# Performance work log

Hardware: AMD Instinct MI355X
Metric: run time of the kernel (lower is better)

## Reference

```python
import jax, jax.numpy as jnp
import numpy as np

B, N = 4, 8192


def setup_inputs() -> dict:
    key = jax.random.key(0)
    k1, k2, k3 = jax.random.split(key, 3)
    pc_pred = jax.random.normal(k1, (B, N, 3), dtype=jnp.float32)
    pc_target = jax.random.normal(k2, (B, N, 3), dtype=jnp.float32)
    fbpp = jax.random.uniform(k3, (B,), dtype=jnp.float32)
    return {"pc_pred": pc_pred, "pc_target": pc_target, "fbpp": fbpp, "lam": 1}


def _chamfer(x, y):
    # x: (B, N, 3), y: (B, M, 3)
    x2 = jnp.sum(x * x, axis=-1)                     # (B, N)
    y2 = jnp.sum(y * y, axis=-1)                     # (B, M)
    xy = jnp.einsum('bnd,bmd->bnm', x, y)            # (B, N, M)
    d2 = jnp.maximum(x2[:, :, None] + y2[:, None, :] - 2.0 * xy, 0.0)
    cham_x = jnp.mean(jnp.min(d2, axis=2), axis=1)   # (B,) pred -> target
    cham_y = jnp.mean(jnp.min(d2, axis=1), axis=1)   # (B,) target -> pred
    return jnp.mean(cham_x + cham_y)                 # scalar (batch mean)


def reference(pc_pred, pc_target, fbpp, lam):
    d = _chamfer(pc_pred, pc_target)
    r = jnp.mean(fbpp)
    return d + lam * r
```

## Files before the change

kernel.cpp:

```cpp
#include <hip/hip_runtime.h>
#include <math.h>


typedef __attribute__((ext_vector_type(8)))  short  short8;
typedef __attribute__((ext_vector_type(16))) float  f32x16;

#define YS      4
#define RPB     256

#define MFMA2(da, db, A, B0, B1) \
    asm("v_mfma_f32_32x32x16_bf16 %0, %2, %3, 0\n\t" \
        "v_mfma_f32_32x32x16_bf16 %1, %2, %4, 0\n\t" \
        "s_nop 7\n\t" \
        "s_nop 7" \
        : "=&v"(da), "=&v"(db) \
        : "v"(A), "v"(B0), "v"(B1))

static inline int roundup_h(int v, int a) { return (v + a - 1) / a * a; }

static __device__ __forceinline__ unsigned short f2bf(float f) {
    union { float f; unsigned int u; } v; v.f = f;
    unsigned int r = v.u + 0x7FFFu + ((v.u >> 16) & 1u);
    return (unsigned short)(r >> 16);
}
static __device__ __forceinline__ float bf2f(unsigned short s) {
    union { unsigned int u; float f; } v; v.u = ((unsigned int)s) << 16;
    return v.f;
}
static __device__ __forceinline__ unsigned int pk2(unsigned short lo,
                                                   unsigned short hi) {
    return (unsigned int)lo | ((unsigned int)hi << 16);
}

static __device__ __forceinline__ float allmin32(float v) {
    union { float f; int i; } u, t;
    u.f = v;
    t.i = __builtin_amdgcn_update_dpp(u.i, u.i, 0xB1, 0xF, 0xF, false);
    u.f = fminf(u.f, t.f);
    t.i = __builtin_amdgcn_update_dpp(u.i, u.i, 0x4E, 0xF, 0xF, false);
    u.f = fminf(u.f, t.f);
    t.i = __builtin_amdgcn_update_dpp(u.i, u.i, 0x124, 0xF, 0xF, false);
    u.f = fminf(u.f, t.f);
    t.i = __builtin_amdgcn_update_dpp(u.i, u.i, 0x128, 0xF, 0xF, false);
    u.f = fminf(u.f, t.f);
    t.i = __builtin_amdgcn_ds_swizzle(u.i, 0x401F);
    u.f = fminf(u.f, t.f);
    return u.f;
}

__global__ __launch_bounds__(256) void pack_kernel(
    const float* __restrict__ pred, const float* __restrict__ targ,
    int B, int N, int M, int NpadP, int NpadT,
    unsigned short* __restrict__ aP, unsigned short* __restrict__ bP,
    unsigned short* __restrict__ aT, unsigned short* __restrict__ bT)
{
    const int padmax = (NpadP > NpadT) ? NpadP : NpadT;
    const int gid = blockIdx.x * 256 + threadIdx.x;
    if (gid >= B * padmax) return;
    const int b = gid / padmax, i = gid - b * padmax;

    for (int cloud = 0; cloud < 2; ++cloud) {
        const int cnt  = cloud ? M : N;
        const int npad = cloud ? NpadT : NpadP;
        if (i >= npad) continue;
        const float* src = (cloud ? targ : pred) +
                           ((size_t)b * cnt + min(i, cnt - 1)) * 3;
        unsigned short* A  = (cloud ? aT : aP) + ((size_t)b * npad + i) * 16;
        unsigned short* Bk = (cloud ? bT : bP) + (size_t)b * npad * 16;

        const float xs[3] = {src[0], src[1], src[2]};
        const float n2 = xs[0]*xs[0] + xs[1]*xs[1] + xs[2]*xs[2];
        unsigned short th[3], tl[3], yh[3], yl[3];
        #pragma unroll
        for (int c = 0; c < 3; ++c) {
            const float t = -2.0f * xs[c];
            th[c] = f2bf(t);     tl[c] = f2bf(t - bf2f(th[c]));
            yh[c] = f2bf(xs[c]); yl[c] = f2bf(xs[c] - bf2f(yh[c]));
        }
        const unsigned short n2h = f2bf(n2);
        const unsigned short n2l = f2bf(n2 - bf2f(n2h));
        const unsigned short ONE = 0x3F80;

        uint4 alo, ahi, blo, bhi;
        alo.x = pk2(th[0], th[1]); alo.y = pk2(th[2], tl[0]);
        alo.z = pk2(tl[1], tl[2]); alo.w = pk2(th[0], th[1]);
        ahi.x = pk2(th[2], tl[0]); ahi.y = pk2(tl[1], tl[2]);
        ahi.z = pk2(ONE,  ONE);    ahi.w = pk2(n2h,  n2l);
        blo.x = pk2(yh[0], yh[1]); blo.y = pk2(yh[2], yh[0]);
        blo.z = pk2(yh[1], yh[2]); blo.w = pk2(yl[0], yl[1]);
        bhi.x = pk2(yl[2], yl[0]); bhi.y = pk2(yl[1], yl[2]);
        bhi.z = pk2(n2h,  n2l);    bhi.w = pk2(ONE,  ONE);

        *(uint4*)(A)     = alo;  *(uint4*)(A + 8) = ahi;
        const size_t tb = (size_t)(i >> 5) * 64 + (i & 31);
        *(uint4*)(Bk + tb * 8)        = blo;
        *(uint4*)(Bk + (tb + 32) * 8) = bhi;
    }
}

__global__ __launch_bounds__(256, 4) void mfma_sweep(
    const unsigned short* __restrict__ aP, const unsigned short* __restrict__ bP,
    const unsigned short* __restrict__ aT, const unsigned short* __restrict__ bT,
    int B, int N, int M, int NpadP, int NpadT, int NpadMax,
    float* __restrict__ rowpart)
{
    const int tid  = threadIdx.x;
    const int w    = tid >> 6;
    const int lane = tid & 63;
    const int lc   = lane & 31, h = lane >> 5;

    const int SP = NpadMax / RPB;
    int t = blockIdx.x;
    const int sp  = t % SP;  t /= SP;
    const int js  = t % YS;  t /= YS;
    const int b   = t % B;   t /= B;
    const int dir = t;

    const unsigned short* Xp = (dir == 0) ? aP : aT;
    const unsigned short* Yp = (dir == 0) ? bT : bP;
    const int NpadX = (dir == 0) ? NpadP : NpadT;
    const int NpadY = (dir == 0) ? NpadT : NpadP;
    const int Nx    = (dir == 0) ? N : M;
    if (sp * RPB >= NpadX) return;

    const int TM  = NpadY / 32;
    const int nt0 = TM / YS;
    const int t0  = js * nt0;

    const int row0 = sp * RPB + w * 64;
    const size_t abase = ((size_t)b * NpadX + row0 + lc) * 16 + (size_t)h * 8;
    const short8 a0 = *reinterpret_cast<const short8*>(Xp + abase);
    const short8 a1 = *reinterpret_cast<const short8*>(Xp + abase + 32 * 16);

    f32x16 rm0, rm1;
    #pragma unroll
    for (int r = 0; r < 16; ++r) {
        rm0[r] = __builtin_inff(); rm1[r] = __builtin_inff();
    }

    const unsigned short* yp =
        Yp + (size_t)b * NpadY * 16 + (size_t)t0 * 512 + (size_t)lane * 8;
    short8 c0 = *reinterpret_cast<const short8*>(yp);
    short8 c1 = *reinterpret_cast<const short8*>(yp + 512);

    for (int j = 0; j < nt0; j += 2) {
        const short8 n0 = *reinterpret_cast<const short8*>(yp + 1024);
        const short8 n1 = *reinterpret_cast<const short8*>(yp + 1536);
        yp += 1024;
        __builtin_amdgcn_sched_barrier(0);
        {
            f32x16 da, db;
            MFMA2(da, db, a0, c0, c1);
            #pragma unroll
            for (int r = 0; r < 16; ++r)
                rm0[r] = fminf(fminf(da[r], db[r]), rm0[r]);
        }
        {
            f32x16 da, db;
            MFMA2(da, db, a1, c0, c1);
            #pragma unroll
            for (int r = 0; r < 16; ++r)
                rm1[r] = fminf(fminf(da[r], db[r]), rm1[r]);
        }
        c0 = n0; c1 = n1;
    }

    const size_t outb = (((size_t)dir * B + b) * YS + js) * (size_t)NpadMax;
    #pragma unroll
    for (int r = 0; r < 16; ++r) {
        const float v0 = allmin32(rm0[r]);
        const float v1 = allmin32(rm1[r]);
        if (lc == 0) {
            const int rr = (r & 3) + 8 * (r >> 2) + 4 * h;
            const int ra = row0 + rr, rb = row0 + 32 + rr;
            if (ra < Nx) rowpart[outb + ra] = v0;
            if (rb < Nx) rowpart[outb + rb] = v1;
        }
    }
}

__global__ __launch_bounds__(256) void combine_kernel(
    const float* __restrict__ rowpart, int B, int N, int M,
    int NpadP, int NpadT, int NpadMax,
    float invBN, float invBM, float* __restrict__ partial)
{
    const int tid = threadIdx.x;
    const int tot = 2 * B * NpadMax;
    float acc = 0.f;
    for (int idx = blockIdx.x * 256 + tid; idx < tot; idx += gridDim.x * 256) {
        const int row = idx % NpadMax;
        const int rem = idx / NpadMax;
        const int b   = rem % B;
        const int dir = rem / B;
        const int Nx  = (dir == 0) ? N : M;
        if (row >= Nx) continue;
        float m = __builtin_inff();
        #pragma unroll
        for (int js = 0; js < YS; ++js)
            m = fminf(m, rowpart[(((size_t)dir * B + b) * YS + js)
                                 * (size_t)NpadMax + row]);
        acc += fmaxf(m, 0.f) * ((dir == 0) ? invBN : invBM);
    }
    __shared__ float sb[256];
    sb[tid] = acc; __syncthreads();
    for (int off2 = 128; off2 > 0; off2 >>= 1) {
        if (tid < off2) sb[tid] += sb[tid + off2];
        __syncthreads();
    }
    if (tid == 0) partial[blockIdx.x] = sb[0];
}

__global__ void finalize_kernel(const float* __restrict__ partial, int np,
                                const float* __restrict__ fbpp, int Bf,
                                const void* __restrict__ lamp,
                                float* __restrict__ out)
{
    __shared__ float sb[256];
    const int tid = threadIdx.x;
    float acc = 0.f;
    for (int i = tid; i < np; i += 256) acc += partial[i];
    sb[tid] = acc;
    __syncthreads();
    for (int off = 128; off > 0; off >>= 1) {
        if (tid < off) sb[tid] += sb[tid + off];
        __syncthreads();
    }
    if (tid == 0) {
        const int li = *(const int*)lamp;
        const float lam = (li >= -1000000 && li <= 1000000)
                            ? (float)li : *(const float*)lamp;
        float fm = 0.f;
        for (int i = 0; i < Bf; ++i) fm += fbpp[i];
        fm /= (float)Bf;
        out[0] = sb[0] + lam * fm;
    }
}

extern "C" void kernel_launch(void* const* d_in, const int* in_sizes, int n_in,
                              void* d_out, int out_size, void* d_ws, size_t ws_size,
                              hipStream_t stream) {
    const float* pred = (const float*)d_in[0];
    const float* targ = (const float*)d_in[1];
    const float* fbpp = (const float*)d_in[2];
    const void*  lamp = d_in[3];

    const int B = in_sizes[2];
    const int N = in_sizes[0] / (3 * B);
    const int M = in_sizes[1] / (3 * B);
    const int NpadP = roundup_h(N, RPB);
    const int NpadT = roundup_h(M, RPB);
    const int NpadMax = (NpadP > NpadT) ? NpadP : NpadT;

    size_t o = 0;
    auto take = [&](size_t bytes) {
        size_t r = o; o += (bytes + 255) & ~(size_t)255; return r;
    };
    unsigned short* aP = (unsigned short*)((char*)d_ws +
                         take((size_t)B * NpadP * 32 + 8192));
    unsigned short* bP = (unsigned short*)((char*)d_ws +
                         take((size_t)B * NpadP * 32 + 8192));
    unsigned short* aT = (unsigned short*)((char*)d_ws +
                         take((size_t)B * NpadT * 32 + 8192));
    unsigned short* bT = (unsigned short*)((char*)d_ws +
                         take((size_t)B * NpadT * 32 + 8192));
    float* rowpart = (float*)((char*)d_ws +
                     take((size_t)2 * B * YS * NpadMax * sizeof(float)));
    float* partial = (float*)((char*)d_ws + take(256 * sizeof(float)));
    (void)ws_size;

    pack_kernel<<<(B * NpadMax + 255) / 256, 256, 0, stream>>>(
        pred, targ, B, N, M, NpadP, NpadT, aP, bP, aT, bT);

    const int SP = NpadMax / RPB;
    const int blocks = 2 * B * YS * SP;
    mfma_sweep<<<blocks, 256, 0, stream>>>(
        aP, bP, aT, bT, B, N, M, NpadP, NpadT, NpadMax, rowpart);

    combine_kernel<<<256, 256, 0, stream>>>(
        rowpart, B, N, M, NpadP, NpadT, NpadMax,
        1.f / ((float)B * (float)N), 1.f / ((float)B * (float)M), partial);

    finalize_kernel<<<1, 256, 0, stream>>>(partial, 256, fbpp, B, lamp,
                                           (float*)d_out);
}
```

Before: 38.85 us.

## Split Y across more blocks and unroll MFMA loop four tiles deep

Doubles the number of Y splits per row block, so each block scans half as many target tiles and the grid grows, raising parallelism across CUs. The inner loop now processes four 32-column tiles per iteration with deeper register prefetching, and remainder loops handle odd tile counts. The cost is more partial-min rows for the combine kernel to reduce and higher register pressure from the extra prefetched operands.

Result: slower. 40.86 us (+5.2%).

```diff
diff --git a/kernel.cpp b/kernel.cpp
--- a/kernel.cpp
+++ b/kernel.cpp
@@ -5,7 +5,7 @@
 typedef __attribute__((ext_vector_type(8)))  short  short8;
 typedef __attribute__((ext_vector_type(16))) float  f32x16;
 
-#define YS      4
+#define YS      8
 #define RPB     256
 
 #define MFMA2(da, db, A, B0, B1) \
@@ -15,6 +15,17 @@
         "s_nop 7" \
         : "=&v"(da), "=&v"(db) \
         : "v"(A), "v"(B0), "v"(B1))
+
+#define WORKPAIR(p0, p1) do { \
+    { f32x16 da, db; MFMA2(da, db, a0, p0, p1); \
+      _Pragma("unroll") \
+      for (int r = 0; r < 16; ++r) \
+          rm0[r] = fminf(fminf(da[r], db[r]), rm0[r]); } \
+    { f32x16 da, db; MFMA2(da, db, a1, p0, p1); \
+      _Pragma("unroll") \
+      for (int r = 0; r < 16; ++r) \
+          rm1[r] = fminf(fminf(da[r], db[r]), rm1[r]); } \
+} while (0)
 
 static inline int roundup_h(int v, int a) { return (v + a - 1) / a * a; }
 
@@ -140,29 +151,37 @@
 
     const unsigned short* yp =
         Yp + (size_t)b * NpadY * 16 + (size_t)t0 * 512 + (size_t)lane * 8;
-    short8 c0 = *reinterpret_cast<const short8*>(yp);
-    short8 c1 = *reinterpret_cast<const short8*>(yp + 512);
-
-    for (int j = 0; j < nt0; j += 2) {
-        const short8 n0 = *reinterpret_cast<const short8*>(yp + 1024);
-        const short8 n1 = *reinterpret_cast<const short8*>(yp + 1536);
+
+    int j = 0;
+    if (nt0 >= 4) {
+        short8 c0 = *reinterpret_cast<const short8*>(yp);
+        short8 c1 = *reinterpret_cast<const short8*>(yp + 512);
+        short8 d0 = *reinterpret_cast<const short8*>(yp + 1024);
+        short8 d1 = *reinterpret_cast<const short8*>(yp + 1536);
+        for (; j + 8 <= nt0; j += 4) {
+            const short8 e0 = *reinterpret_cast<const short8*>(yp + 2048);
+            const short8 e1 = *reinterpret_cast<const short8*>(yp + 2560);
+            const short8 f0 = *reinterpret_cast<const short8*>(yp + 3072);
+            const short8 f1 = *reinterpret_cast<const short8*>(yp + 3584);
+            yp += 2048;
+            __builtin_amdgcn_sched_barrier(0);
+            WORKPAIR(c0, c1);
+            WORKPAIR(d0, d1);
+            c0 = e0; c1 = e1; d0 = f0; d1 = f1;
+        }
+        WORKPAIR(c0, c1);
+        WORKPAIR(d0, d1);
+        j += 4; yp += 2048;
+    }
+    for (; j + 2 <= nt0; j += 2) {
+        const short8 g0 = *reinterpret_cast<const short8*>(yp);
+        const short8 g1 = *reinterpret_cast<const short8*>(yp + 512);
+        WORKPAIR(g0, g1);
         yp += 1024;
-        __builtin_amdgcn_sched_barrier(0);
-        {
-            f32x16 da, db;
-            MFMA2(da, db, a0, c0, c1);
-            #pragma unroll
-            for (int r = 0; r < 16; ++r)
-                rm0[r] = fminf(fminf(da[r], db[r]), rm0[r]);
-        }
-        {
-            f32x16 da, db;
-            MFMA2(da, db, a1, c0, c1);
-            #pragma unroll
-            for (int r = 0; r < 16; ++r)
-                rm1[r] = fminf(fminf(da[r], db[r]), rm1[r]);
-        }
-        c0 = n0; c1 = n1;
+    }
+    if (j < nt0) {
+        const short8 g0 = *reinterpret_cast<const short8*>(yp);
+        WORKPAIR(g0, g0);
     }
 
     const size_t outb = (((size_t)dir * B + b) * YS + js) * (size_t)NpadMax;
```
